# Kernel optimization log

Hardware: AMD Instinct MI355X
Metric: run time of the kernel (lower is better)

## Reference

```python
import jax, jax.numpy as jnp
import numpy as np

B, H, S, DK = 4, 16, 2048, 128
NEG = -1e9  # large-negative stand-in for -inf additive mask
CAUSAL = True  # module constructed with mask=True (decoder self-attention)


def setup_inputs() -> dict:
    key = jax.random.key(0)
    kq, kk, kv, kl = jax.random.split(key, 4)
    q = jax.random.normal(kq, (B, H, S, DK), dtype=jnp.float32)
    k = jax.random.normal(kk, (B, H, S, DK), dtype=jnp.float32)
    v = jax.random.normal(kv, (B, H, S, DK), dtype=jnp.float32)
    sen_len = jax.random.randint(kl, (B,), 1, S + 1, dtype=jnp.int32)
    return {"q": q, "k": k, "v": v, "sen_len": sen_len}


def reference(q, k, v, sen_len):
    # att = q @ k^T / sqrt(d)   -> (B, H, S, S)
    scale = 1.0 / jnp.sqrt(jnp.asarray(DK, dtype=q.dtype))
    att = jnp.einsum('bhqd,bhkd->bhqk', q, k) * scale

    # Fused padding (+ optional causal) mask, multiplicative zero-mask and
    # additive -inf mask, exactly as att*zero_mask + inf_mask in the original.
    pos = jnp.arange(S)
    valid = pos[None, :] < sen_len[:, None]                 # (B, S) token validity
    zmask = (valid[:, :, None] & valid[:, None, :])         # (B, S, S) pad mask
    if CAUSAL:
        zmask = zmask & (pos[None, :, None] >= pos[None, None, :])
    zmask = zmask[:, None, :, :].astype(att.dtype)          # (B, 1, S, S)
    att = att * zmask + NEG * (1.0 - zmask)

    att = jax.nn.softmax(att, axis=-1)
    return jnp.einsum('bhqk,bhkd->bhqd', att, v)
```

## Files before the change

### kernel.cpp

```cpp
#include <hip/hip_runtime.h>
#include <hip/hip_bf16.h>

#define Bb   4
#define Hh   16
#define Ss   2048
#define Dd   128
#define QBLK 128
#define KVB  64

typedef __attribute__((ext_vector_type(8))) short bf16x8;
typedef __attribute__((ext_vector_type(4))) float f32x4;
typedef __attribute__((ext_vector_type(4))) float fvec4;
typedef __attribute__((ext_vector_type(2))) unsigned u32x2;
typedef __attribute__((ext_vector_type(4))) unsigned u32x4;

__device__ __forceinline__ unsigned pk2(float a, float b) {
    __hip_bfloat162 h = __float22bfloat162_rn(make_float2(a, b));
    unsigned u; __builtin_memcpy(&u, &h, 4); return u;
}

typedef const __attribute__((address_space(1))) char* gas_t;
typedef __attribute__((address_space(3))) char* las_t;
__device__ __forceinline__ void gld16(const void* g, void* l) {
    __builtin_amdgcn_global_load_lds((gas_t)g, (las_t)l, 16, 0, 0);
}

__global__ __launch_bounds__(256) void cvtk_kernel(const float* __restrict__ K,
                                                   short* __restrict__ Kb) {
    size_t i = ((size_t)blockIdx.x * 256 + threadIdx.x) * 8;
    fvec4 a = ((const fvec4*)(K + i))[0];
    fvec4 b = ((const fvec4*)(K + i))[1];
    u32x4 u;
    u[0] = pk2(a[0], a[1]); u[1] = pk2(a[2], a[3]);
    u[2] = pk2(b[0], b[1]); u[3] = pk2(b[2], b[3]);
    *(u32x4*)(Kb + i) = u;
}

__global__ __launch_bounds__(256) void cvtv_kernel(const float* __restrict__ V,
                                                   short* __restrict__ Vt,
                                                   float* __restrict__ part) {
    __shared__ short Lt[128 * 136];
    __shared__ fvec4 red[256];
    const int bh = blockIdx.x >> 4, ch = blockIdx.x & 15;
    const int tid = threadIdx.x;
    const float* src = V + ((size_t)bh * Ss + ch * 128) * Dd;
    const int c4 = tid & 31, s0 = tid >> 5;
    fvec4 acc = {0.f, 0.f, 0.f, 0.f};
    #pragma unroll
    for (int i = 0; i < 16; ++i) {
        int s = s0 + 8 * i;
        fvec4 v = ((const fvec4*)(src + (size_t)s * Dd))[c4];
        acc += v;
        u32x2 p; p[0] = pk2(v[0], v[1]); p[1] = pk2(v[2], v[3]);
        *(u32x2*)&Lt[s * 136 + c4 * 4] = p;
    }
    red[tid] = acc;
    __syncthreads();
    for (int off = 128; off >= 32; off >>= 1) {
        if (tid < off) red[tid] += red[tid + off];
        __syncthreads();
    }
    if (tid < 32) ((fvec4*)(part + (size_t)blockIdx.x * Dd))[tid] = red[tid];
    #pragma unroll
    for (int i = 0; i < 8; ++i) {
        int g2 = tid + 256 * i;
        int d = g2 >> 4, sg = g2 & 15;
        short tmp[8];
        #pragma unroll
        for (int j = 0; j < 8; ++j) tmp[j] = Lt[(sg * 8 + j) * 136 + d];
        u32x4 u; __builtin_memcpy(&u, tmp, 16);
        *(u32x4*)(Vt + ((size_t)(bh * Dd + d)) * Ss + ch * 128 + sg * 8) = u;
    }
}

__global__ __launch_bounds__(256) void vpart_kernel(const float* __restrict__ V,
                                                    float* __restrict__ part) {
    int blk = blockIdx.x, bh = blk >> 3, ch = blk & 7;
    int tid = threadIdx.x, d4 = tid & 31, rg = tid >> 5;
    const fvec4* p = (const fvec4*)(V + ((size_t)bh * Ss + ch * 256) * Dd) + d4;
    fvec4 s = {0.f, 0.f, 0.f, 0.f};
    for (int rr = 0; rr < 32; ++rr) s += p[(size_t)(rg * 32 + rr) * 32];
    __shared__ fvec4 red[256];
    red[tid] = s;
    __syncthreads();
    for (int off = 128; off >= 32; off >>= 1) {
        if (tid < off) red[tid] += red[tid + off];
        __syncthreads();
    }
    if (tid < 32) ((fvec4*)(part + (size_t)blk * Dd))[tid] = red[tid];
}

__global__ __launch_bounds__(128) void vcomb_kernel(const float* __restrict__ part,
                                                    float* __restrict__ vm, int nch) {
    int bh = blockIdx.x, d = threadIdx.x;
    float s = 0.f;
    for (int c = 0; c < nch; ++c) s += part[(size_t)(bh * nch + c) * Dd + d];
    vm[bh * Dd + d] = s * (1.0f / 2048.0f);
}

__global__ __launch_bounds__(512, 2) void attn8_kernel(
    const float* __restrict__ Qg, const short* __restrict__ Kbf,
    const short* __restrict__ Vtb, const int* __restrict__ slen,
    const float* __restrict__ vmean, float* __restrict__ Og)
{
    __shared__ __align__(16) char smem[163840];

    const int bid = blockIdx.x;
    const int qslot = bid >> 6, r = bid & 63;
    const int qt = 15 - qslot;
    const int b  = (r >> 3) & 3;
    const int h  = (r & 7) | ((r >> 5) << 3);
    const int bh = b * 16 + h;
    const int len = slen[b];
    const int q0 = qt * QBLK;
    const int tid = threadIdx.x;

    if (q0 >= len) {
        const fvec4* vm4 = (const fvec4*)(vmean + bh * Dd);
        fvec4 val = vm4[tid & 31];
        float* ob = Og + ((size_t)bh * Ss + q0) * Dd;
        int r0 = tid >> 5;
        #pragma unroll
        for (int i = 0; i < 8; ++i)
            ((fvec4*)(ob + (size_t)(r0 + 16 * i) * Dd))[tid & 31] = val;
        return;
    }

    const int w = tid >> 6, lane = tid & 63;
    const int grp = w >> 2, wg = w & 3;
    const int g = lane >> 4, qc = lane & 15;
    const int qw0 = q0 + wg * 32;
    const bool wave_active = (qw0 < len);

    const int kv_end   = min(q0 + QBLK, len);
    const int kv_end_w = min(qw0 + 32, kv_end);
    const int nt  = (kv_end + KVB - 1) >> 6;
    const int itn = (nt + 1) >> 1;

    char* const KgB = smem + grp * 32768;
    char* const VgB = smem + 65536 + grp * 32768;
    char* const PsB = smem + 131072 + w * 4096;

    int CK[4], CV[4];
    const char* KbhB = (const char*)Kbf + (size_t)bh * Ss * 256;
    const char* VbhB = (const char*)Vtb + (size_t)bh * Dd * (Ss * 2);
    #pragma unroll
    for (int i = 0; i < 4; ++i) {
        int krow = wg * 16 + i * 4 + (lane >> 4);
        int jK = lane & 15;
        int jKs = (jK & 8) | ((jK & 7) ^ (krow & 7));
        CK[i] = krow * 256 + jKs * 16;
        int d = wg * 32 + i * 8 + (lane >> 3);
        int jV = lane & 7;
        CV[i] = d * 4096 + (jV ^ (d & 7)) * 16;
    }

    #define GISSUE8(tile_, buf_) do {                                                  \
        size_t kb_ = (size_t)(tile_) * (KVB * 256);                                    \
        size_t vb_ = (size_t)(tile_) * (KVB * 2);                                      \
        _Pragma("unroll")                                                              \
        for (int i_ = 0; i_ < 4; ++i_)                                                 \
            gld16(KbhB + kb_ + CK[i_], KgB + (buf_) * 16384 + wg * 4096 + i_ * 1024);  \
        _Pragma("unroll")                                                              \
        for (int i_ = 0; i_ < 4; ++i_)                                                 \
            gld16(VbhB + vb_ + CV[i_], VgB + (buf_) * 16384 + wg * 4096 + i_ * 1024);  \
    } while (0)

    if (grp < nt) GISSUE8(grp, 0);

    const float SC = 0.12752870368768582f;
    bf16x8 qf[2][4];
    #pragma unroll
    for (int t2 = 0; t2 < 2; ++t2) {
        const float* qrow = Qg + ((size_t)bh * Ss + (qw0 + 16 * t2 + qc)) * Dd;
        #pragma unroll
        for (int kc = 0; kc < 4; ++kc) {
            const fvec4* p = (const fvec4*)(qrow + kc * 32 + g * 8);
            fvec4 a = p[0], bv = p[1];
            unsigned* fu = (unsigned*)&qf[t2][kc];
            fu[0] = pk2(a[0] * SC, a[1] * SC);
            fu[1] = pk2(a[2] * SC, a[3] * SC);
            fu[2] = pk2(bv[0] * SC, bv[1] * SC);
            fu[3] = pk2(bv[2] * SC, bv[3] * SC);
        }
    }

    asm volatile("s_waitcnt vmcnt(0)" ::: "memory");
    __syncthreads();

    f32x4 o[2][8];
    #pragma unroll
    for (int t2 = 0; t2 < 2; ++t2)
        #pragma unroll
        for (int dt = 0; dt < 8; ++dt) o[t2][dt] = (f32x4){0.f, 0.f, 0.f, 0.f};
    float m_[2]   = {-3e38f, -3e38f};
    float lsum[2] = {0.f, 0.f};

    for (int i = 0; i < itn; ++i) {
        const int t = 2 * i + grp;
        const int kv0 = t * KVB;
        const int tn = t + 2;
        const bool active = wave_active && (t < nt) && (kv0 < kv_end_w);

        if (tn < nt) GISSUE8(tn, (i + 1) & 1);

        if (active) {
            const char* KsB = KgB + (i & 1) * 16384;
            const char* VtB = VgB + (i & 1) * 16384;
            f32x4 sa[2][4];
            #pragma unroll
            for (int t2 = 0; t2 < 2; ++t2)
                #pragma unroll
                for (int mt = 0; mt < 4; ++mt) sa[t2][mt] = (f32x4){0.f, 0.f, 0.f, 0.f};
            __builtin_amdgcn_s_setprio(1);
            #pragma unroll
            for (int mt = 0; mt < 4; ++mt) {
                int row = mt * 16 + qc;
                bf16x8 kf[4];
                #pragma unroll
                for (int kc = 0; kc < 4; ++kc) {
                    int jb = kc * 4 + g;
                    int js = (jb & 8) | ((jb & 7) ^ (row & 7));
                    kf[kc] = *(const bf16x8*)(KsB + row * 256 + js * 16);
                }
                #pragma unroll
                for (int t2 = 0; t2 < 2; ++t2)
                    #pragma unroll
                    for (int kc = 0; kc < 4; ++kc)
                        sa[t2][mt] = __builtin_amdgcn_mfma_f32_16x16x32_bf16(
                            kf[kc], qf[t2][kc], sa[t2][mt], 0, 0, 0);
            }
            __builtin_amdgcn_s_setprio(0);

            #pragma unroll
            for (int t2 = 0; t2 < 2; ++t2) {
                const int qrow = qw0 + 16 * t2 + qc;
                const bool full = (kv0 + KVB - 1) <= (qw0 + 16 * t2);
                if (!full) {
                    #pragma unroll
                    for (int mt = 0; mt < 4; ++mt)
                        #pragma unroll
                        for (int rr = 0; rr < 4; ++rr) {
                            int kk = kv0 + mt * 16 + g * 4 + rr;
                            if (kk > qrow) sa[t2][mt][rr] = -3e38f;
                        }
                }
                float tm = sa[t2][0][0];
                #pragma unroll
                for (int mt = 0; mt < 4; ++mt)
                    #pragma unroll
                    for (int rr = 0; rr < 4; ++rr) tm = fmaxf(tm, sa[t2][mt][rr]);
                tm = fmaxf(tm, __shfl_xor(tm, 16));
                tm = fmaxf(tm, __shfl_xor(tm, 32));
                if (__any(tm > m_[t2] + 8.0f)) {
                    float mnew = fmaxf(m_[t2], tm);
                    float al = exp2f(m_[t2] - mnew);
                    m_[t2] = mnew;
                    lsum[t2] *= al;
                    #pragma unroll
                    for (int rr = 0; rr < 4; ++rr) {
                        float alr = __shfl(al, g * 4 + rr);
                        #pragma unroll
                        for (int dt = 0; dt < 8; ++dt) o[t2][dt][rr] *= alr;
                    }
                }
                float mref = m_[t2];
                float ls = 0.f;
                int prow = t2 * 16 + qc;
                int pswz = (prow & 7) << 4;
                #pragma unroll
                for (int mt = 0; mt < 4; ++mt) {
                    f32x4 p;
                    #pragma unroll
                    for (int rr = 0; rr < 4; ++rr)
                        p[rr] = exp2f(sa[t2][mt][rr] - mref);
                    ls += (p[0] + p[1]) + (p[2] + p[3]);
                    u32x2 pw;
                    pw[0] = pk2(p[0], p[1]);
                    pw[1] = pk2(p[2], p[3]);
                    *(u32x2*)(PsB + ((prow * 128 + mt * 32 + g * 8) ^ pswz)) = pw;
                }
                lsum[t2] += ls;
            }

            bf16x8 ap[2][2];
            #pragma unroll
            for (int t2 = 0; t2 < 2; ++t2) {
                int prow = t2 * 16 + qc;
                int pswz = (prow & 7) << 4;
                #pragma unroll
                for (int c = 0; c < 2; ++c)
                    ap[t2][c] = *(const bf16x8*)(PsB + ((prow * 128 + c * 64 + g * 16) ^ pswz));
            }
            __builtin_amdgcn_s_setprio(1);
            #pragma unroll
            for (int dt = 0; dt < 8; ++dt) {
                int d = dt * 16 + qc;
                #pragma unroll
                for (int c = 0; c < 2; ++c) {
                    int js = (c * 4 + g) ^ (d & 7);
                    bf16x8 bfv = *(const bf16x8*)(VtB + d * 128 + js * 16);
                    #pragma unroll
                    for (int t2 = 0; t2 < 2; ++t2)
                        o[t2][dt] = __builtin_amdgcn_mfma_f32_16x16x32_bf16(
                            ap[t2][c], bfv, o[t2][dt], 0, 0, 0);
                }
            }
            __builtin_amdgcn_s_setprio(0);
        }

        asm volatile("s_waitcnt vmcnt(0)" ::: "memory");
        __syncthreads();
    }
    #undef GISSUE8

    __syncthreads();
    float* dumpO  = (float*)smem;
    float* dumpML = (float*)(smem + 65536);
    if (grp == 1) {
        #pragma unroll
        for (int t2 = 0; t2 < 2; ++t2) {
            float L = lsum[t2];
            L += __shfl_xor(L, 16);
            L += __shfl_xor(L, 32);
            if (lane < 16) {
                dumpML[wg * 64 + t2 * 32 + qc * 2 + 0] = m_[t2];
                dumpML[wg * 64 + t2 * 32 + qc * 2 + 1] = L;
            }
            #pragma unroll
            for (int dt = 0; dt < 8; ++dt)
                *(f32x4*)(dumpO + wg * 4096 + (t2 * 8 + dt) * 256 + lane * 4) = o[t2][dt];
        }
    }
    __syncthreads();
    if (grp == 1) return;

    bool needvm = (qw0 + 32 > len);
    float vmv[8];
    #pragma unroll
    for (int dt = 0; dt < 8; ++dt)
        vmv[dt] = needvm ? vmean[bh * Dd + dt * 16 + qc] : 0.f;

    #pragma unroll
    for (int t2 = 0; t2 < 2; ++t2) {
        float mB = dumpML[wg * 64 + t2 * 32 + qc * 2 + 0];
        float lB = dumpML[wg * 64 + t2 * 32 + qc * 2 + 1];
        float LA = lsum[t2];
        LA += __shfl_xor(LA, 16);
        LA += __shfl_xor(LA, 32);
        float mM = fmaxf(m_[t2], mB);
        float aA = exp2f(m_[t2] - mM);
        float aB = exp2f(mB - mM);
        float invL = 1.0f / (LA * aA + lB * aB);
        f32x4 obv[8];
        #pragma unroll
        for (int dt = 0; dt < 8; ++dt)
            obv[dt] = *(const f32x4*)(dumpO + wg * 4096 + (t2 * 8 + dt) * 256 + lane * 4);
        #pragma unroll
        for (int rr = 0; rr < 4; ++rr) {
            float aAr = __shfl(aA, g * 4 + rr);
            float aBr = __shfl(aB, g * 4 + rr);
            float ivr = __shfl(invL, g * 4 + rr);
            int rowg = qw0 + t2 * 16 + g * 4 + rr;
            float* orow = Og + ((size_t)bh * Ss + rowg) * Dd + qc;
            #pragma unroll
            for (int dt = 0; dt < 8; ++dt) {
                float val = (o[t2][dt][rr] * aAr + obv[dt][rr] * aBr) * ivr;
                if (rowg >= len) val = vmv[dt];
                orow[dt * 16] = val;
            }
        }
    }
}

__global__ __launch_bounds__(256, 2) void attn_fb_kernel(
    const float* __restrict__ Qg, const float* __restrict__ Kg,
    const float* __restrict__ Vg, const int* __restrict__ slen,
    const float* __restrict__ vmean, float* __restrict__ Og)
{
    __shared__ __align__(16) short Ks[KVB * Dd];
    __shared__ __align__(16) short Vt[Dd * KVB];
    __shared__ __align__(16) short Ps[4 * 32 * KVB];

    const int bid = blockIdx.x;
    const int qslot = bid >> 6, r = bid & 63;
    const int qt = 15 - qslot;
    const int b  = (r >> 3) & 3;
    const int h  = (r & 7) | ((r >> 5) << 3);
    const int bh = b * 16 + h;
    const int len = slen[b];
    const int q0 = qt * QBLK;
    const int tid = threadIdx.x;

    if (q0 >= len) {
        const fvec4* vm4 = (const fvec4*)(vmean + bh * Dd);
        fvec4 val = vm4[tid & 31];
        float* ob = Og + ((size_t)bh * Ss + q0) * Dd;
        int r0 = tid >> 5;
        #pragma unroll
        for (int i = 0; i < 16; ++i)
            ((fvec4*)(ob + (size_t)(r0 + 8 * i) * Dd))[tid & 31] = val;
        return;
    }

    const int w = tid >> 6, lane = tid & 63;
    const int g = lane >> 4, qc = lane & 15;
    const int qw0 = q0 + w * 32;
    const bool wave_active = (qw0 < len);

    const int kv_end   = min(q0 + QBLK, len);
    const int kv_end_w = min(qw0 + 32, kv_end);
    const int nt = (kv_end + KVB - 1) >> 6;

    const float SC = 0.12752870368768582f;
    bf16x8 qf[2][4];
    #pragma unroll
    for (int t2 = 0; t2 < 2; ++t2) {
        const float* qrow = Qg + ((size_t)bh * Ss + (qw0 + 16 * t2 + qc)) * Dd;
        #pragma unroll
        for (int kc = 0; kc < 4; ++kc) {
            const fvec4* p = (const fvec4*)(qrow + kc * 32 + g * 8);
            fvec4 a = p[0], bv = p[1];
            unsigned* fu = (unsigned*)&qf[t2][kc];
            fu[0] = pk2(a[0] * SC, a[1] * SC);
            fu[1] = pk2(a[2] * SC, a[3] * SC);
            fu[2] = pk2(bv[0] * SC, bv[1] * SC);
            fu[3] = pk2(bv[2] * SC, bv[3] * SC);
        }
    }

    f32x4 o[2][8];
    #pragma unroll
    for (int t2 = 0; t2 < 2; ++t2)
        #pragma unroll
        for (int dt = 0; dt < 8; ++dt) o[t2][dt] = (f32x4){0.f, 0.f, 0.f, 0.f};
    float m_[2]   = {-3e38f, -3e38f};
    float lsum[2] = {0.f, 0.f};
    char* PsB = (char*)Ps + w * 4096;

    for (int t = 0; t < nt; ++t) {
        const int kv0 = t * KVB;
        const bool active = wave_active && (kv0 < kv_end_w);
        __syncthreads();
        {
            const fvec4* sk = (const fvec4*)(Kg + ((size_t)bh * Ss + kv0) * Dd);
            #pragma unroll
            for (int i = 0; i < 8; ++i) {
                int f = tid + 256 * i;
                int kr = f >> 5, d4 = f & 31;
                fvec4 v = sk[(size_t)kr * 32 + d4];
                u32x2 pr; pr[0] = pk2(v[0], v[1]); pr[1] = pk2(v[2], v[3]);
                int j = d4 >> 1;
                int js = (j & 8) | ((j & 7) ^ (kr & 7));
                *(u32x2*)((char*)Ks + kr * 256 + js * 16 + (d4 & 1) * 8) = pr;
            }
            const float* sv = Vg + ((size_t)bh * Ss + kv0) * Dd;
            #pragma unroll
            for (int i = 0; i < 2; ++i) {
                int idx = tid + 256 * i;
                int dt4 = idx & 31, kt4 = idx >> 5;
                fvec4 vv[4];
                #pragma unroll
                for (int jj = 0; jj < 4; ++jj)
                    vv[jj] = ((const fvec4*)(sv + (size_t)(kt4 * 4 + jj) * Dd))[dt4];
                #pragma unroll
                for (int jj = 0; jj < 4; ++jj) {
                    int d = dt4 * 4 + jj;
                    u32x2 pr;
                    pr[0] = pk2(vv[0][jj], vv[1][jj]);
                    pr[1] = pk2(vv[2][jj], vv[3][jj]);
                    int bo = d * 128 + ((kt4 >> 1) ^ (d & 7)) * 16 + (kt4 & 1) * 8;
                    *(u32x2*)((char*)Vt + bo) = pr;
                }
            }
        }
        __syncthreads();

        if (active) {
            f32x4 sa[2][4];
            #pragma unroll
            for (int t2 = 0; t2 < 2; ++t2)
                #pragma unroll
                for (int mt = 0; mt < 4; ++mt) sa[t2][mt] = (f32x4){0.f, 0.f, 0.f, 0.f};
            #pragma unroll
            for (int mt = 0; mt < 4; ++mt) {
                int row = mt * 16 + qc;
                bf16x8 kf[4];
                #pragma unroll
                for (int kc = 0; kc < 4; ++kc) {
                    int jb = kc * 4 + g;
                    int js = (jb & 8) | ((jb & 7) ^ (row & 7));
                    kf[kc] = *(const bf16x8*)((const char*)Ks + row * 256 + js * 16);
                }
                #pragma unroll
                for (int t2 = 0; t2 < 2; ++t2)
                    #pragma unroll
                    for (int kc = 0; kc < 4; ++kc)
                        sa[t2][mt] = __builtin_amdgcn_mfma_f32_16x16x32_bf16(
                            kf[kc], qf[t2][kc], sa[t2][mt], 0, 0, 0);
            }
            #pragma unroll
            for (int t2 = 0; t2 < 2; ++t2) {
                const int qrow = qw0 + 16 * t2 + qc;
                const bool full = (kv0 + KVB - 1) <= (qw0 + 16 * t2);
                if (!full) {
                    #pragma unroll
                    for (int mt = 0; mt < 4; ++mt)
                        #pragma unroll
                        for (int rr = 0; rr < 4; ++rr) {
                            int kk = kv0 + mt * 16 + g * 4 + rr;
                            if (kk > qrow) sa[t2][mt][rr] = -3e38f;
                        }
                }
                float tm = sa[t2][0][0];
                #pragma unroll
                for (int mt = 0; mt < 4; ++mt)
                    #pragma unroll
                    for (int rr = 0; rr < 4; ++rr) tm = fmaxf(tm, sa[t2][mt][rr]);
                tm = fmaxf(tm, __shfl_xor(tm, 16));
                tm = fmaxf(tm, __shfl_xor(tm, 32));
                if (__any(tm > m_[t2] + 8.0f)) {
                    float mnew = fmaxf(m_[t2], tm);
                    float al = exp2f(m_[t2] - mnew);
                    m_[t2] = mnew;
                    lsum[t2] *= al;
                    #pragma unroll
                    for (int rr = 0; rr < 4; ++rr) {
                        float alr = __shfl(al, g * 4 + rr);
                        #pragma unroll
                        for (int dt = 0; dt < 8; ++dt) o[t2][dt][rr] *= alr;
                    }
                }
                float mref = m_[t2];
                float ls = 0.f;
                int prow = t2 * 16 + qc;
                int pswz = (prow & 7) << 4;
                #pragma unroll
                for (int mt = 0; mt < 4; ++mt) {
                    f32x4 p;
                    #pragma unroll
                    for (int rr = 0; rr < 4; ++rr)
                        p[rr] = exp2f(sa[t2][mt][rr] - mref);
                    ls += (p[0] + p[1]) + (p[2] + p[3]);
                    u32x2 pw;
                    pw[0] = pk2(p[0], p[1]);
                    pw[1] = pk2(p[2], p[3]);
                    *(u32x2*)(PsB + ((prow * 128 + mt * 32 + g * 8) ^ pswz)) = pw;
                }
                lsum[t2] += ls;
            }
            bf16x8 ap[2][2];
            #pragma unroll
            for (int t2 = 0; t2 < 2; ++t2) {
                int prow = t2 * 16 + qc;
                int pswz = (prow & 7) << 4;
                #pragma unroll
                for (int c = 0; c < 2; ++c)
                    ap[t2][c] = *(const bf16x8*)(PsB + ((prow * 128 + c * 64 + g * 16) ^ pswz));
            }
            #pragma unroll
            for (int dt = 0; dt < 8; ++dt) {
                int d = dt * 16 + qc;
                #pragma unroll
                for (int c = 0; c < 2; ++c) {
                    int js = (c * 4 + g) ^ (d & 7);
                    bf16x8 bfv = *(const bf16x8*)((const char*)Vt + d * 128 + js * 16);
                    #pragma unroll
                    for (int t2 = 0; t2 < 2; ++t2)
                        o[t2][dt] = __builtin_amdgcn_mfma_f32_16x16x32_bf16(
                            ap[t2][c], bfv, o[t2][dt], 0, 0, 0);
                }
            }
        }
    }

    float inv_[2][4];
    #pragma unroll
    for (int t2 = 0; t2 < 2; ++t2) {
        float L = lsum[t2];
        L += __shfl_xor(L, 16);
        L += __shfl_xor(L, 32);
        #pragma unroll
        for (int rr = 0; rr < 4; ++rr) {
            float Lr = __shfl(L, g * 4 + rr);
            inv_[t2][rr] = 1.0f / Lr;
        }
    }
    bool needvm = (qw0 + 32 > len);
    float vmv[8];
    #pragma unroll
    for (int dt = 0; dt < 8; ++dt)
        vmv[dt] = needvm ? vmean[bh * Dd + dt * 16 + qc] : 0.f;
    #pragma unroll
    for (int t2 = 0; t2 < 2; ++t2)
        #pragma unroll
        for (int rr = 0; rr < 4; ++rr) {
            int rowg = qw0 + t2 * 16 + g * 4 + rr;
            float* orow = Og + ((size_t)bh * Ss + rowg) * Dd + qc;
            #pragma unroll
            for (int dt = 0; dt < 8; ++dt) {
                float val = o[t2][dt][rr] * inv_[t2][rr];
                if (rowg >= len) val = vmv[dt];
                orow[dt * 16] = val;
            }
        }
}

extern "C" void kernel_launch(void* const* d_in, const int* in_sizes, int n_in,
                              void* d_out, int out_size, void* d_ws, size_t ws_size,
                              hipStream_t stream) {
    const float* q  = (const float*)d_in[0];
    const float* k  = (const float*)d_in[1];
    const float* v  = (const float*)d_in[2];
    const int*   sl = (const int*)d_in[3];
    float* out = (float*)d_out;

    const size_t nElem = (size_t)Bb * Hh * Ss * Dd;
    const size_t need0 = nElem * 2 * 2 + 1024 * Dd * 4 + 64 * Dd * 4;

    if (ws_size >= need0) {
        short* Kbf  = (short*)d_ws;
        short* Vtb  = Kbf + nElem;
        float* part = (float*)(Vtb + nElem);
        float* vm   = part + 1024 * Dd;
        cvtk_kernel<<<dim3(8192), dim3(256), 0, stream>>>(k, Kbf);
        cvtv_kernel<<<dim3(1024), dim3(256), 0, stream>>>(v, Vtb, part);
        vcomb_kernel<<<dim3(Bb * Hh), dim3(128), 0, stream>>>(part, vm, 16);
        attn8_kernel<<<dim3(1024), dim3(512), 0, stream>>>(q, Kbf, Vtb, sl, vm, out);
    } else {
        float* part = (float*)d_ws;
        float* vm   = part + 512 * Dd;
        vpart_kernel<<<dim3(512), dim3(256), 0, stream>>>(v, part);
        vcomb_kernel<<<dim3(Bb * Hh), dim3(128), 0, stream>>>(part, vm, 8);
        attn_fb_kernel<<<dim3(1024), dim3(256), 0, stream>>>(q, k, v, sl, vm, out);
    }
}
```

Measured before the change: 154.4 us.

## Pre-swizzle K/V into MFMA fragment order and read directly from global

The conversion kernels now write K and V as bf16 in per-tile MFMA-fragment order, so each lane's operand is one contiguous 16-byte load. The attention kernel drops LDS staging, the global_load_lds double buffering and the barriers. Each 256-thread block has four independent waves that load K/V fragments straight from global/L2, with per-wave causal tile counts. This removes LDS traffic and synchronisation, but K/V reuse across waves now depends on cache hits and there is no explicit prefetch to hide latency.

```diff
diff --git a/kernel.cpp b/kernel.cpp
--- a/kernel.cpp
+++ b/kernel.cpp
@@ -19,58 +19,54 @@
     unsigned u; __builtin_memcpy(&u, &h, 4); return u;
 }
 
-typedef const __attribute__((address_space(1))) char* gas_t;
-typedef __attribute__((address_space(3))) char* las_t;
-__device__ __forceinline__ void gld16(const void* g, void* l) {
-    __builtin_amdgcn_global_load_lds((gas_t)g, (las_t)l, 16, 0, 0);
-}
-
-__global__ __launch_bounds__(256) void cvtk_kernel(const float* __restrict__ K,
-                                                   short* __restrict__ Kb) {
-    size_t i = ((size_t)blockIdx.x * 256 + threadIdx.x) * 8;
-    fvec4 a = ((const fvec4*)(K + i))[0];
-    fvec4 b = ((const fvec4*)(K + i))[1];
-    u32x4 u;
-    u[0] = pk2(a[0], a[1]); u[1] = pk2(a[2], a[3]);
-    u[2] = pk2(b[0], b[1]); u[3] = pk2(b[2], b[3]);
-    *(u32x4*)(Kb + i) = u;
-}
-
-__global__ __launch_bounds__(256) void cvtv_kernel(const float* __restrict__ V,
-                                                   short* __restrict__ Vt,
-                                                   float* __restrict__ part) {
-    __shared__ short Lt[128 * 136];
-    __shared__ fvec4 red[256];
-    const int bh = blockIdx.x >> 4, ch = blockIdx.x & 15;
+__global__ __launch_bounds__(256) void cvtkf_kernel(const float* __restrict__ K,
+                                                    short* __restrict__ Kf) {
+    const int bh = blockIdx.x >> 5, kt = blockIdx.x & 31;
     const int tid = threadIdx.x;
-    const float* src = V + ((size_t)bh * Ss + ch * 128) * Dd;
-    const int c4 = tid & 31, s0 = tid >> 5;
-    fvec4 acc = {0.f, 0.f, 0.f, 0.f};
-    #pragma unroll
-    for (int i = 0; i < 16; ++i) {
-        int s = s0 + 8 * i;
-        fvec4 v = ((const fvec4*)(src + (size_t)s * Dd))[c4];
-        acc += v;
-        u32x2 p; p[0] = pk2(v[0], v[1]); p[1] = pk2(v[2], v[3]);
-        *(u32x2*)&Lt[s * 136 + c4 * 4] = p;
-    }
-    red[tid] = acc;
+    const float* Kb = K + ((size_t)bh * Ss + kt * 64) * Dd;
+    short* out = Kf + ((size_t)(bh * 32 + kt)) * 8192;
+    #pragma unroll
+    for (int i = 0; i < 4; ++i) {
+        int c = tid + 256 * i;
+        int mt = c >> 8, kc = (c >> 6) & 3, l = c & 63;
+        int g = l >> 4, qc = l & 15;
+        const fvec4* p = (const fvec4*)(Kb + (size_t)(mt * 16 + qc) * Dd + kc * 32 + g * 8);
+        fvec4 a = p[0], b = p[1];
+        u32x4 u;
+        u[0] = pk2(a[0], a[1]); u[1] = pk2(a[2], a[3]);
+        u[2] = pk2(b[0], b[1]); u[3] = pk2(b[2], b[3]);
+        *(u32x4*)(out + c * 8) = u;
+    }
+}
+
+__global__ __launch_bounds__(256) void cvtvf_kernel(const float* __restrict__ V,
+                                                    short* __restrict__ Vf,
+                                                    float* __restrict__ part) {
+    __shared__ float bins[128];
+    const int bh = blockIdx.x >> 5, kt = blockIdx.x & 31;
+    const int tid = threadIdx.x;
+    if (tid < 128) bins[tid] = 0.f;
     __syncthreads();
-    for (int off = 128; off >= 32; off >>= 1) {
-        if (tid < off) red[tid] += red[tid + off];
-        __syncthreads();
-    }
-    if (tid < 32) ((fvec4*)(part + (size_t)blockIdx.x * Dd))[tid] = red[tid];
-    #pragma unroll
-    for (int i = 0; i < 8; ++i) {
-        int g2 = tid + 256 * i;
-        int d = g2 >> 4, sg = g2 & 15;
-        short tmp[8];
-        #pragma unroll
-        for (int j = 0; j < 8; ++j) tmp[j] = Lt[(sg * 8 + j) * 136 + d];
-        u32x4 u; __builtin_memcpy(&u, tmp, 16);
-        *(u32x4*)(Vt + ((size_t)(bh * Dd + d)) * Ss + ch * 128 + sg * 8) = u;
-    }
+    const float* Vb = V + ((size_t)bh * Ss + kt * 64) * Dd;
+    short* out = Vf + ((size_t)(bh * 32 + kt)) * 8192;
+    #pragma unroll
+    for (int i = 0; i < 4; ++i) {
+        int c = tid + 256 * i;
+        int dt = c >> 7, cc = (c >> 6) & 1, l = c & 63;
+        int g = l >> 4, qc = l & 15;
+        int d = dt * 16 + qc;
+        const float* src = Vb + (size_t)(cc * 32 + g * 8) * Dd + d;
+        float v[8]; float s = 0.f;
+        #pragma unroll
+        for (int j = 0; j < 8; ++j) { v[j] = src[(size_t)j * Dd]; s += v[j]; }
+        atomicAdd(&bins[d], s);
+        u32x4 u;
+        u[0] = pk2(v[0], v[1]); u[1] = pk2(v[2], v[3]);
+        u[2] = pk2(v[4], v[5]); u[3] = pk2(v[6], v[7]);
+        *(u32x4*)(out + c * 8) = u;
+    }
+    __syncthreads();
+    if (tid < 128) part[(size_t)blockIdx.x * Dd + tid] = bins[tid];
 }
 
 __global__ __launch_bounds__(256) void vpart_kernel(const float* __restrict__ V,
@@ -98,12 +94,211 @@
     vm[bh * Dd + d] = s * (1.0f / 2048.0f);
 }
 
-__global__ __launch_bounds__(512, 2) void attn8_kernel(
-    const float* __restrict__ Qg, const short* __restrict__ Kbf,
-    const short* __restrict__ Vtb, const int* __restrict__ slen,
+__global__ __launch_bounds__(256) void attnw_kernel(
+    const float* __restrict__ Qg, const short* __restrict__ Kf,
+    const short* __restrict__ Vf, const int* __restrict__ slen,
     const float* __restrict__ vmean, float* __restrict__ Og)
 {
-    __shared__ __align__(16) char smem[163840];
+    __shared__ __align__(16) short Ps[4 * 2048];
+
+    const int bid = blockIdx.x;
+    const int qslot = bid >> 6, r = bid & 63;
+    const int qt4 = 15 - qslot;
+    const int b  = (r >> 3) & 3;
+    const int h  = (r & 7) | ((r >> 5) << 3);
+    const int bh = b * 16 + h;
+    const int len = slen[b];
+    const int tid = threadIdx.x;
+    const int w = tid >> 6, lane = tid & 63;
+    const int g = lane >> 4, qc = lane & 15;
+    const int qw0 = qt4 * QBLK + w * 32;
+
+    if (qw0 >= len) {
+        const fvec4* vm4 = (const fvec4*)(vmean + bh * Dd);
+        fvec4 val = vm4[lane & 31];
+        float* ob = Og + ((size_t)bh * Ss + qw0) * Dd;
+        int r0 = lane >> 5;
+        #pragma unroll
+        for (int i = 0; i < 16; ++i)
+            ((fvec4*)(ob + (size_t)(r0 + 2 * i) * Dd))[lane & 31] = val;
+        return;
+    }
+
+    const int kv_end_w = min(qw0 + 32, len);
+    const int nt = (kv_end_w + KVB - 1) >> 6;
+
+    const char* KfB = (const char*)Kf + (size_t)bh * 524288;
+    const char* VfB = (const char*)Vf + (size_t)bh * 524288;
+    const int lo16 = lane * 16;
+
+    const float SC = 0.12752870368768582f;
+    bf16x8 qf[2][4];
+    #pragma unroll
+    for (int t2 = 0; t2 < 2; ++t2) {
+        const float* qrow = Qg + ((size_t)bh * Ss + (qw0 + 16 * t2 + qc)) * Dd;
+        #pragma unroll
+        for (int kc = 0; kc < 4; ++kc) {
+            const fvec4* p = (const fvec4*)(qrow + kc * 32 + g * 8);
+            fvec4 a = p[0], bv = p[1];
+            unsigned* fu = (unsigned*)&qf[t2][kc];
+            fu[0] = pk2(a[0] * SC, a[1] * SC);
+            fu[1] = pk2(a[2] * SC, a[3] * SC);
+            fu[2] = pk2(bv[0] * SC, bv[1] * SC);
+            fu[3] = pk2(bv[2] * SC, bv[3] * SC);
+        }
+    }
+
+    f32x4 o[2][8];
+    #pragma unroll
+    for (int t2 = 0; t2 < 2; ++t2)
+        #pragma unroll
+        for (int dt = 0; dt < 8; ++dt) o[t2][dt] = (f32x4){0.f, 0.f, 0.f, 0.f};
+    float m_[2]   = {-3e38f, -3e38f};
+    float lsum[2] = {0.f, 0.f};
+
+    char* PsB = (char*)Ps + w * 4096;
+
+    for (int t = 0; t < nt; ++t) {
+        const int kv0 = t * KVB;
+        const char* Ktile = KfB + (size_t)t * 16384;
+        const char* Vtile = VfB + (size_t)t * 16384;
+
+        f32x4 sa[2][4];
+        #pragma unroll
+        for (int t2 = 0; t2 < 2; ++t2)
+            #pragma unroll
+            for (int mt = 0; mt < 4; ++mt) sa[t2][mt] = (f32x4){0.f, 0.f, 0.f, 0.f};
+        __builtin_amdgcn_s_setprio(1);
+        #pragma unroll
+        for (int mt = 0; mt < 4; ++mt) {
+            bf16x8 kf[4];
+            #pragma unroll
+            for (int kc = 0; kc < 4; ++kc)
+                kf[kc] = *(const bf16x8*)(Ktile + (mt * 4 + kc) * 1024 + lo16);
+            #pragma unroll
+            for (int t2 = 0; t2 < 2; ++t2)
+                #pragma unroll
+                for (int kc = 0; kc < 4; ++kc)
+                    sa[t2][mt] = __builtin_amdgcn_mfma_f32_16x16x32_bf16(
+                        kf[kc], qf[t2][kc], sa[t2][mt], 0, 0, 0);
+        }
+        __builtin_amdgcn_s_setprio(0);
+
+        #pragma unroll
+        for (int t2 = 0; t2 < 2; ++t2) {
+            const int qrow = qw0 + 16 * t2 + qc;
+            const bool full = (kv0 + KVB - 1) <= (qw0 + 16 * t2);
+            if (!full) {
+                #pragma unroll
+                for (int mt = 0; mt < 4; ++mt)
+                    #pragma unroll
+                    for (int rr = 0; rr < 4; ++rr) {
+                        int kk = kv0 + mt * 16 + g * 4 + rr;
+                        if (kk > qrow) sa[t2][mt][rr] = -3e38f;
+                    }
+            }
+            float tm = sa[t2][0][0];
+            #pragma unroll
+            for (int mt = 0; mt < 4; ++mt)
+                #pragma unroll
+                for (int rr = 0; rr < 4; ++rr) tm = fmaxf(tm, sa[t2][mt][rr]);
+            tm = fmaxf(tm, __shfl_xor(tm, 16));
+            tm = fmaxf(tm, __shfl_xor(tm, 32));
+            if (__any(tm > m_[t2] + 8.0f)) {
+                float mnew = fmaxf(m_[t2], tm);
+                float al = exp2f(m_[t2] - mnew);
+                m_[t2] = mnew;
+                lsum[t2] *= al;
+                #pragma unroll
+                for (int rr = 0; rr < 4; ++rr) {
+                    float alr = __shfl(al, g * 4 + rr);
+                    #pragma unroll
+                    for (int dt = 0; dt < 8; ++dt) o[t2][dt][rr] *= alr;
+                }
+            }
+            float mref = m_[t2];
+            float ls = 0.f;
+            int prow = t2 * 16 + qc;
+            int pswz = (prow & 7) << 4;
+            #pragma unroll
+            for (int mt = 0; mt < 4; ++mt) {
+                f32x4 p;
+                #pragma unroll
+                for (int rr = 0; rr < 4; ++rr)
+                    p[rr] = exp2f(sa[t2][mt][rr] - mref);
+                ls += (p[0] + p[1]) + (p[2] + p[3]);
+                u32x2 pw;
+                pw[0] = pk2(p[0], p[1]);
+                pw[1] = pk2(p[2], p[3]);
+                *(u32x2*)(PsB + ((prow * 128 + mt * 32 + g * 8) ^ pswz)) = pw;
+            }
+            lsum[t2] += ls;
+        }
+
+        bf16x8 ap[2][2];
+        #pragma unroll
+        for (int t2 = 0; t2 < 2; ++t2) {
+            int prow = t2 * 16 + qc;
+            int pswz = (prow & 7) << 4;
+            #pragma unroll
+            for (int c = 0; c < 2; ++c)
+                ap[t2][c] = *(const bf16x8*)(PsB + ((prow * 128 + c * 64 + g * 16) ^ pswz));
+        }
+        __builtin_amdgcn_s_setprio(1);
+        #pragma unroll
+        for (int dt = 0; dt < 8; ++dt) {
+            #pragma unroll
+            for (int cc = 0; cc < 2; ++cc) {
+                bf16x8 bfv = *(const bf16x8*)(Vtile + (dt * 2 + cc) * 1024 + lo16);
+                #pragma unroll
+                for (int t2 = 0; t2 < 2; ++t2)
+                    o[t2][dt] = __builtin_amdgcn_mfma_f32_16x16x32_bf16(
+                        ap[t2][cc], bfv, o[t2][dt], 0, 0, 0);
+            }
+        }
+        __builtin_amdgcn_s_setprio(0);
+    }
+
+    float inv_[2][4];
+    #pragma unroll
+    for (int t2 = 0; t2 < 2; ++t2) {
+        float L = lsum[t2];
+        L += __shfl_xor(L, 16);
+        L += __shfl_xor(L, 32);
+        #pragma unroll
+        for (int rr = 0; rr < 4; ++rr) {
+            float Lr = __shfl(L, g * 4 + rr);
+            inv_[t2][rr] = 1.0f / Lr;
+        }
+    }
+    bool needvm = (qw0 + 32 > len);
+    float vmv[8];
+    #pragma unroll
+    for (int dt = 0; dt < 8; ++dt)
+        vmv[dt] = needvm ? vmean[bh * Dd + dt * 16 + qc] : 0.f;
+    #pragma unroll
+    for (int t2 = 0; t2 < 2; ++t2)
+        #pragma unroll
+        for (int rr = 0; rr < 4; ++rr) {
+            int rowg = qw0 + t2 * 16 + g * 4 + rr;
+            float* orow = Og + ((size_t)bh * Ss + rowg) * Dd + qc;
+            #pragma unroll
+            for (int dt = 0; dt < 8; ++dt) {
+                float val = o[t2][dt][rr] * inv_[t2][rr];
+                if (rowg >= len) val = vmv[dt];
+                orow[dt * 16] = val;
+            }
+        }
+}
+
+__global__ __launch_bounds__(256, 2) void attn_fb_kernel(
+    const float* __restrict__ Qg, const float* __restrict__ Kg,
+    const float* __restrict__ Vg, const int* __restrict__ slen,
+    const float* __restrict__ vmean, float* __restrict__ Og)
+{
+    __shared__ __align__(16) short Ks[KVB * Dd];
+    __shared__ __align__(16) short Vt[Dd * KVB];
+    __shared__ __align__(16) short Ps[4 * 32 * KVB];
 
     const int bid = blockIdx.x;
     const int qslot = bid >> 6, r = bid & 63;
@@ -121,52 +316,19 @@
         float* ob = Og + ((size_t)bh * Ss + q0) * Dd;
         int r0 = tid >> 5;
         #pragma unroll
-        for (int i = 0; i < 8; ++i)
-            ((fvec4*)(ob + (size_t)(r0 + 16 * i) * Dd))[tid & 31] = val;
+        for (int i = 0; i < 16; ++i)
+            ((fvec4*)(ob + (size_t)(r0 + 8 * i) * Dd))[tid & 31] = val;
         return;
     }
 
     const int w = tid >> 6, lane = tid & 63;
-    const int grp = w >> 2, wg = w & 3;
     const int g = lane >> 4, qc = lane & 15;
-    const int qw0 = q0 + wg * 32;
+    const int qw0 = q0 + w * 32;
     const bool wave_active = (qw0 < len);
 
     const int kv_end   = min(q0 + QBLK, len);
     const int kv_end_w = min(qw0 + 32, kv_end);
-    const int nt  = (kv_end + KVB - 1) >> 6;
-    const int itn = (nt + 1) >> 1;
-
-    char* const KgB = smem + grp * 32768;
-    char* const VgB = smem + 65536 + grp * 32768;
-    char* const PsB = smem + 131072 + w * 4096;
-
-    int CK[4], CV[4];
-    const char* KbhB = (const char*)Kbf + (size_t)bh * Ss * 256;
-    const char* VbhB = (const char*)Vtb + (size_t)bh * Dd * (Ss * 2);
-    #pragma unroll
-    for (int i = 0; i < 4; ++i) {
-        int krow = wg * 16 + i * 4 + (lane >> 4);
-        int jK = lane & 15;
-        int jKs = (jK & 8) | ((jK & 7) ^ (krow & 7));
-        CK[i] = krow * 256 + jKs * 16;
-        int d = wg * 32 + i * 8 + (lane >> 3);
-        int jV = lane & 7;
-        CV[i] = d * 4096 + (jV ^ (d & 7)) * 16;
-    }
-
-    #define GISSUE8(tile_, buf_) do {                                                  \
-        size_t kb_ = (size_t)(tile_) * (KVB * 256);                                    \
-        size_t vb_ = (size_t)(tile_) * (KVB * 2);                                      \
-        _Pragma("unroll")                                                              \
-        for (int i_ = 0; i_ < 4; ++i_)                                                 \
-            gld16(KbhB + kb_ + CK[i_], KgB + (buf_) * 16384 + wg * 4096 + i_ * 1024);  \
-        _Pragma("unroll")                                                              \
-        for (int i_ = 0; i_ < 4; ++i_)                                                 \
-            gld16(VbhB + vb_ + CV[i_], VgB + (buf_) * 16384 + wg * 4096 + i_ * 1024);  \
-    } while (0)
-
-    if (grp < nt) GISSUE8(grp, 0);
+    const int nt = (kv_end + KVB - 1) >> 6;
 
     const float SC = 0.12752870368768582f;
     bf16x8 qf[2][4];
@@ -185,9 +347,6 @@
         }
     }
 
-    asm volatile("s_waitcnt vmcnt(0)" ::: "memory");
-    __syncthreads();
-
     f32x4 o[2][8];
     #pragma unroll
     for (int t2 = 0; t2 < 2; ++t2)
@@ -195,24 +354,52 @@
         for (int dt = 0; dt < 8; ++dt) o[t2][dt] = (f32x4){0.f, 0.f, 0.f, 0.f};
     float m_[2]   = {-3e38f, -3e38f};
     float lsum[2] = {0.f, 0.f};
-
-    for (int i = 0; i < itn; ++i) {
-        const int t = 2 * i + grp;
+    char* PsB = (char*)Ps + w * 4096;
+
+    for (int t = 0; t < nt; ++t) {
         const int kv0 = t * KVB;
-        const int tn = t + 2;
-        const bool active = wave_active && (t < nt) && (kv0 < kv_end_w);
-
-        if (tn < nt) GISSUE8(tn, (i + 1) & 1);
+        const bool active = wave_active && (kv0 < kv_end_w);
+        __syncthreads();
+        {
+            const fvec4* sk = (const fvec4*)(Kg + ((size_t)bh * Ss + kv0) * Dd);
+            #pragma unroll
+            for (int i = 0; i < 8; ++i) {
+                int f = tid + 256 * i;
+                int kr = f >> 5, d4 = f & 31;
+                fvec4 v = sk[(size_t)kr * 32 + d4];
+                u32x2 pr; pr[0] = pk2(v[0], v[1]); pr[1] = pk2(v[2], v[3]);
+                int j = d4 >> 1;
+                int js = (j & 8) | ((j & 7) ^ (kr & 7));
+                *(u32x2*)((char*)Ks + kr * 256 + js * 16 + (d4 & 1) * 8) = pr;
+            }
+            const float* sv = Vg + ((size_t)bh * Ss + kv0) * Dd;
+            #pragma unroll
+            for (int i = 0; i < 2; ++i) {
+                int idx = tid + 256 * i;
+                int dt4 = idx & 31, kt4 = idx >> 5;
+                fvec4 vv[4];
+                #pragma unroll
+                for (int jj = 0; jj < 4; ++jj)
+                    vv[jj] = ((const fvec4*)(sv + (size_t)(kt4 * 4 + jj) * Dd))[dt4];
+                #pragma unroll
+                for (int jj = 0; jj < 4; ++jj) {
+                    int d = dt4 * 4 + jj;
+                    u32x2 pr;
+                    pr[0] = pk2(vv[0][jj], vv[1][jj]);
+                    pr[1] = pk2(vv[2][jj], vv[3][jj]);
+                    int bo = d * 128 + ((kt4 >> 1) ^ (d & 7)) * 16 + (kt4 & 1) * 8;
+                    *(u32x2*)((char*)Vt + bo) = pr;
+                }
+            }
+        }
+        __syncthreads();
 
         if (active) {
-            const char* KsB = KgB + (i & 1) * 16384;
-            const char* VtB = VgB + (i & 1) * 16384;
             f32x4 sa[2][4];
             #pragma unroll
             for (int t2 = 0; t2 < 2; ++t2)
                 #pragma unroll
                 for (int mt = 0; mt < 4; ++mt) sa[t2][mt] = (f32x4){0.f, 0.f, 0.f, 0.f};
-            __builtin_amdgcn_s_setprio(1);
             #pragma unroll
             for (int mt = 0; mt < 4; ++mt) {
                 int row = mt * 16 + qc;
@@ -221,7 +408,7 @@
                 for (int kc = 0; kc < 4; ++kc) {
                     int jb = kc * 4 + g;
                     int js = (jb & 8) | ((jb & 7) ^ (row & 7));
-                    kf[kc] = *(const bf16x8*)(KsB + row * 256 + js * 16);
+                    kf[kc] = *(const bf16x8*)((const char*)Ks + row * 256 + js * 16);
                 }
                 #pragma unroll
                 for (int t2 = 0; t2 < 2; ++t2)
@@ -230,8 +417,6 @@
                         sa[t2][mt] = __builtin_amdgcn_mfma_f32_16x16x32_bf16(
                             kf[kc], qf[t2][kc], sa[t2][mt], 0, 0, 0);
             }
-            __builtin_amdgcn_s_setprio(0);
-
             #pragma unroll
             for (int t2 = 0; t2 < 2; ++t2) {
                 const int qrow = qw0 + 16 * t2 + qc;
@@ -282,273 +467,6 @@
                 }
                 lsum[t2] += ls;
             }
-
-            bf16x8 ap[2][2];
-            #pragma unroll
-            for (int t2 = 0; t2 < 2; ++t2) {
-                int prow = t2 * 16 + qc;
-                int pswz = (prow & 7) << 4;
-                #pragma unroll
-                for (int c = 0; c < 2; ++c)
-                    ap[t2][c] = *(const bf16x8*)(PsB + ((prow * 128 + c * 64 + g * 16) ^ pswz));
-            }
-            __builtin_amdgcn_s_setprio(1);
-            #pragma unroll
-            for (int dt = 0; dt < 8; ++dt) {
-                int d = dt * 16 + qc;
-                #pragma unroll
-                for (int c = 0; c < 2; ++c) {
-                    int js = (c * 4 + g) ^ (d & 7);
-                    bf16x8 bfv = *(const bf16x8*)(VtB + d * 128 + js * 16);
-                    #pragma unroll
-                    for (int t2 = 0; t2 < 2; ++t2)
-                        o[t2][dt] = __builtin_amdgcn_mfma_f32_16x16x32_bf16(
-                            ap[t2][c], bfv, o[t2][dt], 0, 0, 0);
-                }
-            }
-            __builtin_amdgcn_s_setprio(0);
-        }
-
-        asm volatile("s_waitcnt vmcnt(0)" ::: "memory");
-        __syncthreads();
-    }
-    #undef GISSUE8
-
-    __syncthreads();
-    float* dumpO  = (float*)smem;
-    float* dumpML = (float*)(smem + 65536);
-    if (grp == 1) {
-        #pragma unroll
-        for (int t2 = 0; t2 < 2; ++t2) {
-            float L = lsum[t2];
-            L += __shfl_xor(L, 16);
-            L += __shfl_xor(L, 32);
-            if (lane < 16) {
-                dumpML[wg * 64 + t2 * 32 + qc * 2 + 0] = m_[t2];
-                dumpML[wg * 64 + t2 * 32 + qc * 2 + 1] = L;
-            }
-            #pragma unroll
-            for (int dt = 0; dt < 8; ++dt)
-                *(f32x4*)(dumpO + wg * 4096 + (t2 * 8 + dt) * 256 + lane * 4) = o[t2][dt];
-        }
-    }
-    __syncthreads();
-    if (grp == 1) return;
-
-    bool needvm = (qw0 + 32 > len);
-    float vmv[8];
-    #pragma unroll
-    for (int dt = 0; dt < 8; ++dt)
-        vmv[dt] = needvm ? vmean[bh * Dd + dt * 16 + qc] : 0.f;
-
-    #pragma unroll
-    for (int t2 = 0; t2 < 2; ++t2) {
-        float mB = dumpML[wg * 64 + t2 * 32 + qc * 2 + 0];
-        float lB = dumpML[wg * 64 + t2 * 32 + qc * 2 + 1];
-        float LA = lsum[t2];
-        LA += __shfl_xor(LA, 16);
-        LA += __shfl_xor(LA, 32);
-        float mM = fmaxf(m_[t2], mB);
-        float aA = exp2f(m_[t2] - mM);
-        float aB = exp2f(mB - mM);
-        float invL = 1.0f / (LA * aA + lB * aB);
-        f32x4 obv[8];
-        #pragma unroll
-        for (int dt = 0; dt < 8; ++dt)
-            obv[dt] = *(const f32x4*)(dumpO + wg * 4096 + (t2 * 8 + dt) * 256 + lane * 4);
-        #pragma unroll
-        for (int rr = 0; rr < 4; ++rr) {
-            float aAr = __shfl(aA, g * 4 + rr);
-            float aBr = __shfl(aB, g * 4 + rr);
-            float ivr = __shfl(invL, g * 4 + rr);
-            int rowg = qw0 + t2 * 16 + g * 4 + rr;
-            float* orow = Og + ((size_t)bh * Ss + rowg) * Dd + qc;
-            #pragma unroll
-            for (int dt = 0; dt < 8; ++dt) {
-                float val = (o[t2][dt][rr] * aAr + obv[dt][rr] * aBr) * ivr;
-                if (rowg >= len) val = vmv[dt];
-                orow[dt * 16] = val;
-            }
-        }
-    }
-}
-
-__global__ __launch_bounds__(256, 2) void attn_fb_kernel(
-    const float* __restrict__ Qg, const float* __restrict__ Kg,
-    const float* __restrict__ Vg, const int* __restrict__ slen,
-    const float* __restrict__ vmean, float* __restrict__ Og)
-{
-    __shared__ __align__(16) short Ks[KVB * Dd];
-    __shared__ __align__(16) short Vt[Dd * KVB];
-    __shared__ __align__(16) short Ps[4 * 32 * KVB];
-
-    const int bid = blockIdx.x;
-    const int qslot = bid >> 6, r = bid & 63;
-    const int qt = 15 - qslot;
-    const int b  = (r >> 3) & 3;
-    const int h  = (r & 7) | ((r >> 5) << 3);
-    const int bh = b * 16 + h;
-    const int len = slen[b];
-    const int q0 = qt * QBLK;
-    const int tid = threadIdx.x;
-
-    if (q0 >= len) {
-        const fvec4* vm4 = (const fvec4*)(vmean + bh * Dd);
-        fvec4 val = vm4[tid & 31];
-        float* ob = Og + ((size_t)bh * Ss + q0) * Dd;
-        int r0 = tid >> 5;
-        #pragma unroll
-        for (int i = 0; i < 16; ++i)
-            ((fvec4*)(ob + (size_t)(r0 + 8 * i) * Dd))[tid & 31] = val;
-        return;
-    }
-
-    const int w = tid >> 6, lane = tid & 63;
-    const int g = lane >> 4, qc = lane & 15;
-    const int qw0 = q0 + w * 32;
-    const bool wave_active = (qw0 < len);
-
-    const int kv_end   = min(q0 + QBLK, len);
-    const int kv_end_w = min(qw0 + 32, kv_end);
-    const int nt = (kv_end + KVB - 1) >> 6;
-
-    const float SC = 0.12752870368768582f;
-    bf16x8 qf[2][4];
-    #pragma unroll
-    for (int t2 = 0; t2 < 2; ++t2) {
-        const float* qrow = Qg + ((size_t)bh * Ss + (qw0 + 16 * t2 + qc)) * Dd;
-        #pragma unroll
-        for (int kc = 0; kc < 4; ++kc) {
-            const fvec4* p = (const fvec4*)(qrow + kc * 32 + g * 8);
-            fvec4 a = p[0], bv = p[1];
-            unsigned* fu = (unsigned*)&qf[t2][kc];
-            fu[0] = pk2(a[0] * SC, a[1] * SC);
-            fu[1] = pk2(a[2] * SC, a[3] * SC);
-            fu[2] = pk2(bv[0] * SC, bv[1] * SC);
-            fu[3] = pk2(bv[2] * SC, bv[3] * SC);
-        }
-    }
-
-    f32x4 o[2][8];
-    #pragma unroll
-    for (int t2 = 0; t2 < 2; ++t2)
-        #pragma unroll
-        for (int dt = 0; dt < 8; ++dt) o[t2][dt] = (f32x4){0.f, 0.f, 0.f, 0.f};
-    float m_[2]   = {-3e38f, -3e38f};
-    float lsum[2] = {0.f, 0.f};
-    char* PsB = (char*)Ps + w * 4096;
-
-    for (int t = 0; t < nt; ++t) {
-        const int kv0 = t * KVB;
-        const bool active = wave_active && (kv0 < kv_end_w);
-        __syncthreads();
-        {
-            const fvec4* sk = (const fvec4*)(Kg + ((size_t)bh * Ss + kv0) * Dd);
-            #pragma unroll
-            for (int i = 0; i < 8; ++i) {
-                int f = tid + 256 * i;
-                int kr = f >> 5, d4 = f & 31;
-                fvec4 v = sk[(size_t)kr * 32 + d4];
-                u32x2 pr; pr[0] = pk2(v[0], v[1]); pr[1] = pk2(v[2], v[3]);
-                int j = d4 >> 1;
-                int js = (j & 8) | ((j & 7) ^ (kr & 7));
-                *(u32x2*)((char*)Ks + kr * 256 + js * 16 + (d4 & 1) * 8) = pr;
-            }
-            const float* sv = Vg + ((size_t)bh * Ss + kv0) * Dd;
-            #pragma unroll
-            for (int i = 0; i < 2; ++i) {
-                int idx = tid + 256 * i;
-                int dt4 = idx & 31, kt4 = idx >> 5;
-                fvec4 vv[4];
-                #pragma unroll
-                for (int jj = 0; jj < 4; ++jj)
-                    vv[jj] = ((const fvec4*)(sv + (size_t)(kt4 * 4 + jj) * Dd))[dt4];
-                #pragma unroll
-                for (int jj = 0; jj < 4; ++jj) {
-                    int d = dt4 * 4 + jj;
-                    u32x2 pr;
-                    pr[0] = pk2(vv[0][jj], vv[1][jj]);
-                    pr[1] = pk2(vv[2][jj], vv[3][jj]);
-                    int bo = d * 128 + ((kt4 >> 1) ^ (d & 7)) * 16 + (kt4 & 1) * 8;
-                    *(u32x2*)((char*)Vt + bo) = pr;
-                }
-            }
-        }
-        __syncthreads();
-
-        if (active) {
-            f32x4 sa[2][4];
-            #pragma unroll
-            for (int t2 = 0; t2 < 2; ++t2)
-                #pragma unroll
-                for (int mt = 0; mt < 4; ++mt) sa[t2][mt] = (f32x4){0.f, 0.f, 0.f, 0.f};
-            #pragma unroll
-            for (int mt = 0; mt < 4; ++mt) {
-                int row = mt * 16 + qc;
-                bf16x8 kf[4];
-                #pragma unroll
-                for (int kc = 0; kc < 4; ++kc) {
-                    int jb = kc * 4 + g;
-                    int js = (jb & 8) | ((jb & 7) ^ (row & 7));
-                    kf[kc] = *(const bf16x8*)((const char*)Ks + row * 256 + js * 16);
-                }
-                #pragma unroll
-                for (int t2 = 0; t2 < 2; ++t2)
-                    #pragma unroll
-                    for (int kc = 0; kc < 4; ++kc)
-                        sa[t2][mt] = __builtin_amdgcn_mfma_f32_16x16x32_bf16(
-                            kf[kc], qf[t2][kc], sa[t2][mt], 0, 0, 0);
-            }
-            #pragma unroll
-            for (int t2 = 0; t2 < 2; ++t2) {
-                const int qrow = qw0 + 16 * t2 + qc;
-                const bool full = (kv0 + KVB - 1) <= (qw0 + 16 * t2);
-                if (!full) {
-                    #pragma unroll
-                    for (int mt = 0; mt < 4; ++mt)
-                        #pragma unroll
-                        for (int rr = 0; rr < 4; ++rr) {
-                            int kk = kv0 + mt * 16 + g * 4 + rr;
-                            if (kk > qrow) sa[t2][mt][rr] = -3e38f;
-                        }
-                }
-                float tm = sa[t2][0][0];
-                #pragma unroll
-                for (int mt = 0; mt < 4; ++mt)
-                    #pragma unroll
-                    for (int rr = 0; rr < 4; ++rr) tm = fmaxf(tm, sa[t2][mt][rr]);
-                tm = fmaxf(tm, __shfl_xor(tm, 16));
-                tm = fmaxf(tm, __shfl_xor(tm, 32));
-                if (__any(tm > m_[t2] + 8.0f)) {
-                    float mnew = fmaxf(m_[t2], tm);
-                    float al = exp2f(m_[t2] - mnew);
-                    m_[t2] = mnew;
-                    lsum[t2] *= al;
-                    #pragma unroll
-                    for (int rr = 0; rr < 4; ++rr) {
-                        float alr = __shfl(al, g * 4 + rr);
-                        #pragma unroll
-                        for (int dt = 0; dt < 8; ++dt) o[t2][dt][rr] *= alr;
-                    }
-                }
-                float mref = m_[t2];
-                float ls = 0.f;
-                int prow = t2 * 16 + qc;
-                int pswz = (prow & 7) << 4;
-                #pragma unroll
-                for (int mt = 0; mt < 4; ++mt) {
-                    f32x4 p;
-                    #pragma unroll
-                    for (int rr = 0; rr < 4; ++rr)
-                        p[rr] = exp2f(sa[t2][mt][rr] - mref);
-                    ls += (p[0] + p[1]) + (p[2] + p[3]);
-                    u32x2 pw;
-                    pw[0] = pk2(p[0], p[1]);
-                    pw[1] = pk2(p[2], p[3]);
-                    *(u32x2*)(PsB + ((prow * 128 + mt * 32 + g * 8) ^ pswz)) = pw;
-                }
-                lsum[t2] += ls;
-            }
             bf16x8 ap[2][2];
             #pragma unroll
             for (int t2 = 0; t2 < 2; ++t2) {
@@ -616,17 +534,17 @@
     float* out = (float*)d_out;
 
     const size_t nElem = (size_t)Bb * Hh * Ss * Dd;
-    const size_t need0 = nElem * 2 * 2 + 1024 * Dd * 4 + 64 * Dd * 4;
+    const size_t need0 = nElem * 2 * 2 + 2048 * Dd * 4 + 64 * Dd * 4;
 
     if (ws_size >= need0) {
-        short* Kbf  = (short*)d_ws;
-        short* Vtb  = Kbf + nElem;
-        float* part = (float*)(Vtb + nElem);
-        float* vm   = part + 1024 * Dd;
-        cvtk_kernel<<<dim3(8192), dim3(256), 0, stream>>>(k, Kbf);
-        cvtv_kernel<<<dim3(1024), dim3(256), 0, stream>>>(v, Vtb, part);
-        vcomb_kernel<<<dim3(Bb * Hh), dim3(128), 0, stream>>>(part, vm, 16);
-        attn8_kernel<<<dim3(1024), dim3(512), 0, stream>>>(q, Kbf, Vtb, sl, vm, out);
+        short* Kf   = (short*)d_ws;
+        short* Vf   = Kf + nElem;
+        float* part = (float*)(Vf + nElem);
+        float* vm   = part + 2048 * Dd;
+        cvtkf_kernel<<<dim3(2048), dim3(256), 0, stream>>>(k, Kf);
+        cvtvf_kernel<<<dim3(2048), dim3(256), 0, stream>>>(v, Vf, part);
+        vcomb_kernel<<<dim3(Bb * Hh), dim3(128), 0, stream>>>(part, vm, 32);
+        attnw_kernel<<<dim3(1024), dim3(256), 0, stream>>>(q, Kf, Vf, sl, vm, out);
     } else {
         float* part = (float*)d_ws;
         float* vm   = part + 512 * Dd;
```

Result: slower. 264.3 us (+71.2%).
